# Kernel optimization log

Measured on AMD Instinct MI355X. Metric: run time of the kernel, lower is better.

## Reference

```python
import jax, jax.numpy as jnp
import numpy as np

N, L, K, DROP = 4096, 128, 16, 1
LEFT = N - L * DROP  # 3968


def setup_inputs() -> dict:
    rng = np.random.RandomState(0)
    X = rng.randn(N, N).astype(np.float32)
    A = (X + X.T) / 2.0  # symmetric, like a graph Laplacian
    active = np.ones(N, dtype=bool)
    sel = np.zeros((L, K), dtype=np.int32)
    drp = np.zeros((L, DROP), dtype=np.int32)
    Os = np.zeros((L, K, K), dtype=np.float32)
    for l in range(L):
        cand = np.flatnonzero(active)
        idx = np.sort(rng.choice(cand, size=K, replace=False)).astype(np.int32)
        sel[l] = idx
        drp[l] = idx[:DROP]
        active[idx[:DROP]] = False
        Q, _ = np.linalg.qr(rng.randn(K, K))  # orthogonal init (eigvecs in original)
        Os[l] = Q.astype(np.float32)
    active_idx = np.flatnonzero(active).astype(np.int32)      # (LEFT,) sorted
    inactive_idx = np.flatnonzero(~active).astype(np.int32)   # (N-LEFT,) sorted
    return {
        'A': jnp.asarray(A),
        'Os': jnp.asarray(Os),
        'sel_idx': jnp.asarray(sel),
        'drop_idx': jnp.asarray(drp),
        'active_idx': jnp.asarray(active_idx),
        'inactive_idx': jnp.asarray(inactive_idx),
    }


def reference(A, Os, sel_idx, drop_idx, active_idx, inactive_idx):
    # U_l = I_N with the K x K orthogonal block O_l scattered at (sel, sel).
    # U A U^T therefore only changes K rows and K columns -> rank-K update,
    # identical math to the original dense torch.matmul(U, A) @ U.T.
    n = A.shape[0]
    right0 = jnp.eye(n, dtype=A.dtype)

    def step(carry, xs):
        A_l, right = carry
        O, sel, drp = xs
        A_l = A_l.at[sel, :].set(O @ A_l[sel, :])          # (U A): K rows change
        A_l = A_l.at[:, sel].set(A_l[:, sel] @ O.T)        # (. U^T): K cols change
        right = right.at[sel, :].set(O @ right[sel, :])    # right = U @ right
        wavelet = A_l[drp, :]                              # (drop, N)
        return (A_l, right), wavelet

    (A_L, right), wavelets = jax.lax.scan(step, (A, right0), (Os, sel_idx, drop_idx))
    # wavelets: (L, drop, N)

    active = jnp.zeros((n,), A.dtype).at[active_idx].set(1.0)
    # left_index = eye - diag(diag(outer)) + outer, with outer = active x active
    mask = jnp.eye(n, dtype=A.dtype) - jnp.diag(active) + jnp.outer(active, active)
    D = A_L * mask
    core_wavelets = A_L[active_idx, :]          # (LEFT, N), sorted active order
    mother_wavelets_2 = right[inactive_idx, :]  # (N-LEFT, N)
    father_wavelets_2 = right[active_idx, :]    # (LEFT, N)
    A_rec = right.T @ D @ right
    return A_rec, D, wavelets, core_wavelets, mother_wavelets_2, father_wavelets_2
```

## Files before the change

kernel.cpp:

```cpp
#include <hip/hip_runtime.h>
#include <hip/hip_bf16.h>
#include <stdint.h>

#define N 4096
#define TC 2048
#define LSTEPS 128
#define KSEL 16
#define NACT 3968
#define NIN 128

typedef __hip_bfloat16 bf16;
typedef __attribute__((ext_vector_type(8))) short short8;
typedef __attribute__((ext_vector_type(4))) float floatx4;

static __device__ __forceinline__ bf16 f2bf(float x) { return __float2bfloat16(x); }
static __device__ __forceinline__ float us2f(ushort u) { return __uint_as_float(((unsigned)u) << 16); }
static __device__ __forceinline__ ushort f2us(float x) { return __bfloat16_as_ushort(__float2bfloat16(x)); }

__global__ void prep_kernel(const int* __restrict__ act, const int* __restrict__ inact,
                            int* __restrict__ flags, int* __restrict__ rank) {
    int i = blockIdx.x * blockDim.x + threadIdx.x;
    if (i >= N) return;
    int lo = 0, hi = NACT - 1, f = 0, r = -1;
    while (lo <= hi) {
        int mid = (lo + hi) >> 1, v = act[mid];
        if (v == i) { f = 1; r = mid; break; }
        if (v < i) lo = mid + 1; else hi = mid - 1;
    }
    if (!f) {
        lo = 0; hi = NIN - 1;
        while (lo <= hi) {
            int mid = (lo + hi) >> 1, v = inact[mid];
            if (v == i) { r = mid; break; }
            if (v < i) lo = mid + 1; else hi = mid - 1;
        }
    }
    flags[i] = f;
    rank[i] = r;
}

__global__ __launch_bounds__(1024) void touched_kernel(const int* __restrict__ sel,
                                                       int* __restrict__ tlist,
                                                       int* __restrict__ tpos,
                                                       int* __restrict__ tflag,
                                                       int* __restrict__ selc) {
    __shared__ int flag[N];
    __shared__ int cpos[N];
    __shared__ int wsum[16];
    __shared__ int woff[16];
    __shared__ int s_tau;
    const int t = threadIdx.x;
#pragma unroll
    for (int k = 0; k < 4; k++) flag[t + 1024 * k] = 0;
    __syncthreads();
    flag[sel[t]] = 1;
    flag[sel[t + 1024]] = 1;
    __syncthreads();
    const int b0 = t * 4;
    const int a0 = flag[b0], a1 = flag[b0 + 1], a2 = flag[b0 + 2], a3 = flag[b0 + 3];
    const int s = a0 + a1 + a2 + a3;
    const int lane = t & 63, wv = t >> 6;
    int sc = s;
    for (int off = 1; off < 64; off <<= 1) {
        int o = __shfl_up(sc, off);
        if (lane >= off) sc += o;
    }
    if (lane == 63) wsum[wv] = sc;
    __syncthreads();
    if (t == 0) {
        int acc = 0;
        for (int i = 0; i < 16; i++) { woff[i] = acc; acc += wsum[i]; }
        s_tau = acc;
    }
    __syncthreads();
    const int tau = s_tau;
    const int need = TC - tau;
    int tp = woff[wv] + (sc - s);
    const int aa[4] = {a0, a1, a2, a3};
#pragma unroll
    for (int k = 0; k < 4; k++) {
        const int i = b0 + k;
        int ci;
        if (aa[k]) { ci = tp; tp++; }
        else {
            const int ur = i - tp;
            ci = (ur < need) ? (tau + ur) : -1;
        }
        cpos[i] = ci;
        tpos[i] = ci;
        tflag[i] = (ci >= 0) ? 1 : 0;
        if (ci >= 0) tlist[ci] = i;
    }
    __syncthreads();
    selc[t] = cpos[sel[t]];
    selc[t + 1024] = cpos[sel[t + 1024]];
}

__global__ __launch_bounds__(64) void rscanc_kernel(const float* __restrict__ Os,
                                                    const int* __restrict__ selc,
                                                    bf16* __restrict__ Rct) {
    __shared__ float slab[TC * 4];
    const int t = threadIdx.x;
    const int cc = t & 3;
    const int a = t >> 2;
    const int c0 = blockIdx.x * 4;

    for (int r = t; r < TC * 4; r += 64) slab[r] = 0.0f;
    __syncthreads();
    if (t < 4) slab[(c0 + t) * 4 + t] = 1.0f;
    __syncthreads();

    int selr[16];
    float orow[16];
#pragma unroll
    for (int i = 0; i < 16; i++) selr[i] = selc[i];
#pragma unroll
    for (int i = 0; i < 16; i++) orow[i] = Os[a * 16 + i];

    for (int l = 0; l < LSTEPS; l++) {
        float p[16];
#pragma unroll
        for (int i = 0; i < 16; i++) p[i] = slab[selr[i] * 4 + cc];
#pragma unroll
        for (int i = 0; i < 16; i++) p[i] *= orow[i];
        const float s0 = (p[0] + p[1]) + (p[2] + p[3]);
        const float s1 = (p[4] + p[5]) + (p[6] + p[7]);
        const float s2 = (p[8] + p[9]) + (p[10] + p[11]);
        const float s3 = (p[12] + p[13]) + (p[14] + p[15]);
        const float v = (s0 + s1) + (s2 + s3);
        const int wrow = selr[a];
        int seln[16] = {0};
        float orown[16] = {0.f};
        if (l + 1 < LSTEPS) {
#pragma unroll
            for (int i = 0; i < 16; i++) seln[i] = selc[(l + 1) * 16 + i];
#pragma unroll
            for (int i = 0; i < 16; i++) orown[i] = Os[(l + 1) * 256 + a * 16 + i];
        }
        __syncthreads();
        slab[wrow * 4 + cc] = v;
        __syncthreads();
#pragma unroll
        for (int i = 0; i < 16; i++) { selr[i] = seln[i]; orow[i] = orown[i]; }
    }

    for (int ccw = 0; ccw < 4; ccw++) {
        bf16* dst = Rct + (size_t)(c0 + ccw) * TC;
        for (int r = t; r < TC; r += 64) dst[r] = f2bf(slab[r * 4 + ccw]);
    }
}

__global__ __launch_bounds__(256) void transB_kernel(const bf16* __restrict__ src,
                                                     bf16* __restrict__ dst,
                                                     int R, int C) {
    __shared__ ushort tile[64][65];
    const int t = threadIdx.x;
    const int bx = blockIdx.x, by = blockIdx.y;
    const int tr = t >> 4;
    const int tc = (t & 15) * 4;
#pragma unroll
    for (int k = 0; k < 4; k++) {
        int r = tr + 16 * k;
        const ushort* s = (const ushort*)src + (size_t)(by * 64 + r) * C + bx * 64 + tc;
        ushort4 v = *(const ushort4*)s;
        tile[r][tc + 0] = v.x; tile[r][tc + 1] = v.y;
        tile[r][tc + 2] = v.z; tile[r][tc + 3] = v.w;
    }
    __syncthreads();
#pragma unroll
    for (int k = 0; k < 4; k++) {
        int r = tr + 16 * k;
        ushort4 w;
        w.x = tile[tc + 0][r];
        w.y = tile[tc + 1][r];
        w.z = tile[tc + 2][r];
        w.w = tile[tc + 3][r];
        *(ushort4*)((ushort*)dst + (size_t)(bx * 64 + r) * R + by * 64 + tc) = w;
    }
}

__global__ __launch_bounds__(256) void transF_kernel(const float* __restrict__ src,
                                                     float* __restrict__ dst,
                                                     int R, int C) {
    __shared__ float tile[64][65];
    const int t = threadIdx.x;
    const int bx = blockIdx.x, by = blockIdx.y;
    const int tr = t >> 4;
    const int tc = (t & 15) * 4;
#pragma unroll
    for (int k = 0; k < 4; k++) {
        int r = tr + 16 * k;
        const float* s = src + (size_t)(by * 64 + r) * C + bx * 64 + tc;
        float4 v = *(const float4*)s;
        tile[r][tc + 0] = v.x; tile[r][tc + 1] = v.y;
        tile[r][tc + 2] = v.z; tile[r][tc + 3] = v.w;
    }
    __syncthreads();
#pragma unroll
    for (int k = 0; k < 4; k++) {
        int r = tr + 16 * k;
        float4 w;
        w.x = tile[tc + 0][r];
        w.y = tile[tc + 1][r];
        w.z = tile[tc + 2][r];
        w.w = tile[tc + 3][r];
        *(float4*)(dst + (size_t)(bx * 64 + r) * R + by * 64 + tc) = w;
    }
}

__global__ __launch_bounds__(256) void gatherAt_kernel(const float* __restrict__ A,
                                                       const int* __restrict__ tlist,
                                                       bf16* __restrict__ At) {
    const int r = blockIdx.y;
    const int j0 = (blockIdx.x * 256 + threadIdx.x) * 4;
    const float4 v = *(const float4*)(A + (size_t)tlist[r] * N + j0);
    ushort4 o;
    o.x = f2us(v.x); o.y = f2us(v.y); o.z = f2us(v.z); o.w = f2us(v.w);
    *(ushort4*)((ushort*)At + (size_t)r * N + j0) = o;
}

__global__ __launch_bounds__(256) void gatherRowsB_kernel(const bf16* __restrict__ src,
                                                          const int* __restrict__ tlist,
                                                          bf16* __restrict__ dst) {
    const int r = blockIdx.y;
    const int c0 = (blockIdx.x * 256 + threadIdx.x) * 4;
    ushort4 v = *(const ushort4*)((const ushort*)src + (size_t)tlist[r] * TC + c0);
    *(ushort4*)((ushort*)dst + (size_t)r * TC + c0) = v;
}

__global__ __launch_bounds__(256) void gatherRd_kernel(const bf16* __restrict__ Rc,
                                                       const int* __restrict__ tpos,
                                                       const int* __restrict__ drp,
                                                       bf16* __restrict__ Rd) {
    const int l = blockIdx.y;
    const int c0 = (blockIdx.x * 256 + threadIdx.x) * 4;
    const int pr = tpos[drp[l]];
    ushort4 v = *(const ushort4*)((const ushort*)Rc + (size_t)pr * TC + c0);
    *(ushort4*)((ushort*)Rd + (size_t)l * TC + c0) = v;
}

__global__ __launch_bounds__(256) void gatherColsB_kernel(const bf16* __restrict__ Dt,
                                                          const int* __restrict__ tlist,
                                                          bf16* __restrict__ Dc) {
    const int r = blockIdx.y;
    const int c = blockIdx.x * 256 + threadIdx.x;
    ((ushort*)Dc)[(size_t)r * TC + c] = ((const ushort*)Dt)[(size_t)r * N + tlist[c]];
}

__global__ __launch_bounds__(256) void assembleY_kernel(bf16* __restrict__ Y,
                                                        const bf16* __restrict__ C,
                                                        const int* __restrict__ tflag,
                                                        const int* __restrict__ tpos) {
    const int r = blockIdx.y;
    const int j0 = (blockIdx.x * 256 + threadIdx.x) * 4;
    ushort4 v = *(const ushort4*)((const ushort*)Y + (size_t)r * N + j0);
    const int4 tf = *(const int4*)(tflag + j0);
    const int4 tp = *(const int4*)(tpos + j0);
    const ushort* crow = (const ushort*)C + (size_t)r * TC;
    if (tf.x) v.x = crow[tp.x];
    if (tf.y) v.y = crow[tp.y];
    if (tf.z) v.z = crow[tp.z];
    if (tf.w) v.w = crow[tp.w];
    *(ushort4*)((ushort*)Y + (size_t)r * N + j0) = v;
}

template <bool F32OUT>
__global__ __launch_bounds__(512) void gemmk_kernel(const bf16* __restrict__ Amat, int lda,
                                                    const bf16* __restrict__ Bt, int ldb,
                                                    void* __restrict__ Cv, int ldc, int K) {
    __shared__ bf16 lds[4][(128 + 256) * 32];

    const int t = threadIdx.x;
    const int lane = t & 63;
    const int wave = t >> 6;
    const int wm = wave >> 2;
    const int wn = wave & 3;
    const int rowBase = blockIdx.y * 128;
    const int colBase = blockIdx.x * 256;

    const int sr = lane >> 2;
    const int sgo = (((lane & 3) ^ ((lane >> 3) & 3)) << 3);

    const int frow = lane & 15;
    const int fslot = (((lane >> 4) ^ ((lane >> 1) & 3)) << 4);
    const int aoff0 = (wm * 64 + frow) * 64 + fslot;
    const int boff0 = 128 * 64 + (wn * 64 + frow) * 64 + fslot;

    floatx4 acc[4][4] = {};

#define GK_STAGE_A(bufIdx, kk0)                                                                    \
    do {                                                                                           \
        const bf16* g_ = Amat + (size_t)(rowBase + wave * 16 + sr) * lda + (kk0) + sgo;            \
        char* l_ = (char*)&lds[bufIdx][0] + wave * 1024;                                           \
        __builtin_amdgcn_global_load_lds((const __attribute__((address_space(1))) void*)g_,        \
                                         (__attribute__((address_space(3))) void*)l_, 16, 0, 0);   \
    } while (0)
#define GK_STAGE_B(bufIdx, kk0)                                                                    \
    do {                                                                                           \
        const bf16* g0_ = Bt + (size_t)(colBase + wave * 32 + sr) * ldb + (kk0) + sgo;             \
        const bf16* g1_ = g0_ + (size_t)16 * ldb;                                                  \
        char* l0_ = (char*)&lds[bufIdx][128 * 32] + wave * 2048;                                   \
        __builtin_amdgcn_global_load_lds((const __attribute__((address_space(1))) void*)g0_,       \
                                         (__attribute__((address_space(3))) void*)l0_, 16, 0, 0);  \
        __builtin_amdgcn_global_load_lds((const __attribute__((address_space(1))) void*)g1_,       \
                                         (__attribute__((address_space(3))) void*)(l0_ + 1024),    \
                                         16, 0, 0);                                                \
    } while (0)

    const int NT = K >> 5;
#pragma unroll
    for (int p = 0; p < 3; p++) {
        GK_STAGE_A(p, p * 32);
        GK_STAGE_B(p, p * 32);
    }
    asm volatile("s_waitcnt vmcnt(6)" ::: "memory");
    __builtin_amdgcn_s_barrier();

    for (int tt = 0; tt < NT; tt++) {
        const int buf = tt & 3;
        const char* lA = (const char*)&lds[buf][0];
        const int nbuf = (tt + 3) & 3;
        const bool pf = (tt + 3) < NT;
        const int nk0 = (tt + 3) * 32;

        if (pf) GK_STAGE_A(nbuf, nk0);
        short8 af[4], bfv[4];
#pragma unroll
        for (int mi = 0; mi < 4; mi++) af[mi] = *(const short8*)(lA + aoff0 + mi * 1024);
#pragma unroll
        for (int ni = 0; ni < 2; ni++) bfv[ni] = *(const short8*)(lA + boff0 + ni * 1024);
        __builtin_amdgcn_s_barrier();
        asm volatile("s_waitcnt lgkmcnt(0)" ::: "memory");
        __builtin_amdgcn_s_setprio(1);
#pragma unroll
        for (int mi = 0; mi < 4; mi++)
#pragma unroll
            for (int ni = 0; ni < 2; ni++)
                acc[mi][ni] =
                    __builtin_amdgcn_mfma_f32_16x16x32_bf16(af[mi], bfv[ni], acc[mi][ni], 0, 0, 0);
        __builtin_amdgcn_s_setprio(0);
        __builtin_amdgcn_s_barrier();

        if (pf) GK_STAGE_B(nbuf, nk0);
#pragma unroll
        for (int ni = 2; ni < 4; ni++) bfv[ni] = *(const short8*)(lA + boff0 + ni * 1024);
        __builtin_amdgcn_s_barrier();
        asm volatile("s_waitcnt lgkmcnt(0)" ::: "memory");
        __builtin_amdgcn_s_setprio(1);
#pragma unroll
        for (int mi = 0; mi < 4; mi++)
#pragma unroll
            for (int ni = 2; ni < 4; ni++)
                acc[mi][ni] =
                    __builtin_amdgcn_mfma_f32_16x16x32_bf16(af[mi], bfv[ni], acc[mi][ni], 0, 0, 0);
        __builtin_amdgcn_s_setprio(0);
        asm volatile("s_waitcnt vmcnt(6)" ::: "memory");
        __builtin_amdgcn_s_barrier();
    }
#undef GK_STAGE_A
#undef GK_STAGE_B

    const int crow = (lane >> 4) * 4;
    const int ccol = lane & 15;
    const int rb = rowBase + wm * 64;
    const int cb = colBase + wn * 64;
#pragma unroll
    for (int mi = 0; mi < 4; mi++)
#pragma unroll
        for (int ni = 0; ni < 4; ni++)
#pragma unroll
            for (int r = 0; r < 4; r++) {
                const int gr = rb + mi * 16 + crow + r;
                const int gc = cb + ni * 16 + ccol;
                if (F32OUT)
                    ((float*)Cv)[(size_t)gr * ldc + gc] = acc[mi][ni][r];
                else
                    ((bf16*)Cv)[(size_t)gr * ldc + gc] = f2bf(acc[mi][ni][r]);
            }
}

__global__ __launch_bounds__(256) void maskcore2_kernel(const float* __restrict__ A,
                                                        const bf16* __restrict__ Z,
                                                        const bf16* __restrict__ Zt,
                                                        const int* __restrict__ flags,
                                                        const int* __restrict__ rank,
                                                        const int* __restrict__ tflag,
                                                        const int* __restrict__ tpos,
                                                        float* __restrict__ Dout,
                                                        bf16* __restrict__ Dt,
                                                        float* __restrict__ core) {
    const int i = blockIdx.y;
    const int j0 = (blockIdx.x * 256 + threadIdx.x) * 4;
    const int fi = flags[i];
    const int ri = rank[i];
    const int ti = tflag[i];
    const int pi = tpos[i];
    float4 vf;
    if (ti) {
        const ushort4 v16 = *(const ushort4*)((const ushort*)Z + (size_t)pi * N + j0);
        vf.x = us2f(v16.x); vf.y = us2f(v16.y); vf.z = us2f(v16.z); vf.w = us2f(v16.w);
    } else {
        vf = *(const float4*)(A + (size_t)i * N + j0);
        const int4 tf = *(const int4*)(tflag + j0);
        const int4 tp = *(const int4*)(tpos + j0);
        const ushort* zrow = (const ushort*)Zt + (size_t)i * TC;
        if (tf.x) vf.x = us2f(zrow[tp.x]);
        if (tf.y) vf.y = us2f(zrow[tp.y]);
        if (tf.z) vf.z = us2f(zrow[tp.z]);
        if (tf.w) vf.w = us2f(zrow[tp.w]);
    }
    if (fi) *(float4*)(core + (size_t)ri * N + j0) = vf;
    const int4 fj = *(const int4*)(flags + j0);
    const bool k0 = (i == j0 + 0) || (fi && fj.x);
    const bool k1 = (i == j0 + 1) || (fi && fj.y);
    const bool k2 = (i == j0 + 2) || (fi && fj.z);
    const bool k3 = (i == j0 + 3) || (fi && fj.w);
    float4 df;
    df.x = k0 ? vf.x : 0.0f; df.y = k1 ? vf.y : 0.0f;
    df.z = k2 ? vf.z : 0.0f; df.w = k3 ? vf.w : 0.0f;
    *(float4*)(Dout + (size_t)i * N + j0) = df;
    if (ti) {
        ushort4 dv;
        dv.x = k0 ? f2us(vf.x) : (ushort)0;
        dv.y = k1 ? f2us(vf.y) : (ushort)0;
        dv.z = k2 ? f2us(vf.z) : (ushort)0;
        dv.w = k3 ? f2us(vf.w) : (ushort)0;
        *(ushort4*)((ushort*)Dt + (size_t)pi * N + j0) = dv;
    }
}

__global__ __launch_bounds__(64) void wavelet_kernel(const bf16* __restrict__ Scw,
                                                     const float* __restrict__ Os,
                                                     const int* __restrict__ sel,
                                                     float* __restrict__ wout) {
    __shared__ float u[N];
    const int t = threadIdx.x;
    const int l = blockIdx.x;
    const ushort* src = (const ushort*)(Scw + (size_t)l * N);
    for (int j = t; j < N; j += 64) u[j] = us2f(src[j]);
    __syncthreads();
    for (int m = 0; m <= l; m++) {
        float v = 0.0f;
        int wrow = 0;
        if (t < 16) {
            float p[16];
#pragma unroll
            for (int i = 0; i < 16; i++) p[i] = u[sel[m * 16 + i]];
#pragma unroll
            for (int i = 0; i < 16; i++) p[i] *= Os[m * 256 + t * 16 + i];
            const float s0 = (p[0] + p[1]) + (p[2] + p[3]);
            const float s1 = (p[4] + p[5]) + (p[6] + p[7]);
            const float s2 = (p[8] + p[9]) + (p[10] + p[11]);
            const float s3 = (p[12] + p[13]) + (p[14] + p[15]);
            v = (s0 + s1) + (s2 + s3);
            wrow = sel[m * 16 + t];
        }
        __syncthreads();
        if (t < 16) u[wrow] = v;
        __syncthreads();
    }
    float* dst = wout + (size_t)l * N;
    for (int j = t; j < N; j += 64) dst[j] = u[j];
}

__global__ __launch_bounds__(256) void rowgatherR2_kernel(const bf16* __restrict__ Rc,
                                                          const int* __restrict__ flags,
                                                          const int* __restrict__ rank,
                                                          const int* __restrict__ tflag,
                                                          const int* __restrict__ tpos,
                                                          float* __restrict__ father,
                                                          float* __restrict__ mother) {
    const int i = blockIdx.x;
    const int t = threadIdx.x;
    float* dst = flags[i] ? (father + (size_t)rank[i] * N) : (mother + (size_t)rank[i] * N);
    const int ti = tflag[i];
    const ushort* rrow = (const ushort*)Rc + (size_t)(ti ? tpos[i] : 0) * TC;
    for (int it = 0; it < 4; it++) {
        const int j0 = (it * 256 + t) * 4;
        const int4 tf = *(const int4*)(tflag + j0);
        const int4 tp = *(const int4*)(tpos + j0);
        float4 o;
        o.x = tf.x ? (ti ? us2f(rrow[tp.x]) : 0.f) : ((j0 + 0 == i) ? 1.f : 0.f);
        o.y = tf.y ? (ti ? us2f(rrow[tp.y]) : 0.f) : ((j0 + 1 == i) ? 1.f : 0.f);
        o.z = tf.z ? (ti ? us2f(rrow[tp.z]) : 0.f) : ((j0 + 2 == i) ? 1.f : 0.f);
        o.w = tf.w ? (ti ? us2f(rrow[tp.w]) : 0.f) : ((j0 + 3 == i) ? 1.f : 0.f);
        *(float4*)(dst + j0) = o;
    }
}

__global__ __launch_bounds__(256) void arec_kernel(const float* __restrict__ W,
                                                   const float* __restrict__ Wt,
                                                   const float* __restrict__ D,
                                                   const int* __restrict__ tflag,
                                                   const int* __restrict__ tpos,
                                                   float* __restrict__ Arec) {
    const int i = blockIdx.y;
    const int j0 = (blockIdx.x * 256 + threadIdx.x) * 4;
    float4 o;
    if (tflag[i]) {
        o = *(const float4*)(W + (size_t)tpos[i] * N + j0);
    } else {
        o = *(const float4*)(D + (size_t)i * N + j0);
        const int4 tf = *(const int4*)(tflag + j0);
        const int4 tp = *(const int4*)(tpos + j0);
        const float* wrow = Wt + (size_t)i * TC;
        if (tf.x) o.x = wrow[tp.x];
        if (tf.y) o.y = wrow[tp.y];
        if (tf.z) o.z = wrow[tp.z];
        if (tf.w) o.w = wrow[tp.w];
    }
    *(float4*)(Arec + (size_t)i * N + j0) = o;
}

extern "C" void kernel_launch(void* const* d_in, const int* in_sizes, int n_in,
                              void* d_out, int out_size, void* d_ws, size_t ws_size,
                              hipStream_t stream) {
    const float* A = (const float*)d_in[0];
    const float* Os = (const float*)d_in[1];
    const int* sel = (const int*)d_in[2];
    const int* drp = (const int*)d_in[3];
    const int* act = (const int*)d_in[4];
    const int* inact = (const int*)d_in[5];

    float* out = (float*)d_out;
    float* out_Arec = out;
    float* out_D    = out + 16777216;
    float* out_wav  = out + 33554432;
    float* out_core = out + 34078720;
    float* out_moth = out + 50331648;
    float* out_fath = out + 50855936;

    char* ws = (char*)d_ws;
    const size_t KB = 1024;
    const size_t MB = 1024 * 1024;
    int* tlist = (int*)(ws + 0);
    int* tpos  = (int*)(ws + 64 * KB);
    int* tflag = (int*)(ws + 128 * KB);
    int* selc  = (int*)(ws + 192 * KB);
    int* flags = (int*)(ws + 256 * KB);
    int* rank  = (int*)(ws + 320 * KB);
    bf16* Rd128 = (bf16*)(ws + 512 * KB);
    bf16* Scw   = (bf16*)(ws + 1 * MB);
    bf16* At    = (bf16*)(ws + 2 * MB);
    bf16* At_T  = (bf16*)(ws + 18 * MB);
    bf16* C2    = (bf16*)(ws + 18 * MB);
    bf16* Zt    = (bf16*)(ws + 18 * MB);
    bf16* Rct   = (bf16*)(ws + 34 * MB);
    bf16* Rc    = (bf16*)(ws + 42 * MB);
    bf16* Ac    = (bf16*)(ws + 50 * MB);
    bf16* Y_T   = (bf16*)(ws + 50 * MB);
    float* W    = (float*)(ws + 50 * MB);
    float* Wt   = (float*)(ws + 2 * MB);
    bf16* Y  = At;
    bf16* Z  = At;
    bf16* Dt   = (bf16*)out_Arec;
    bf16* Dc   = (bf16*)((char*)out_Arec + 16 * MB);
    bf16* C4   = (bf16*)((char*)out_Arec + 24 * MB);
    bf16* Y2   = Dt;
    bf16* Y2_T = (bf16*)((char*)out_Arec + 32 * MB);

    prep_kernel<<<dim3(16), dim3(256), 0, stream>>>(act, inact, flags, rank);
    touched_kernel<<<dim3(1), dim3(1024), 0, stream>>>(sel, tlist, tpos, tflag, selc);
    gatherAt_kernel<<<dim3(4, TC), dim3(256), 0, stream>>>(A, tlist, At);
    rscanc_kernel<<<dim3(TC / 4), dim3(64), 0, stream>>>(Os, selc, Rct);
    transB_kernel<<<dim3(32, 32), dim3(256), 0, stream>>>(Rct, Rc, TC, TC);
    transB_kernel<<<dim3(64, 32), dim3(256), 0, stream>>>(At, At_T, TC, N);
    gatherRd_kernel<<<dim3(2, 128), dim3(256), 0, stream>>>(Rc, tpos, drp, Rd128);
    gemmk_kernel<false><<<dim3(16, 1), dim3(512), 0, stream>>>(Rd128, TC, At_T, TC, Scw, N, TC);
    gatherRowsB_kernel<<<dim3(2, TC), dim3(256), 0, stream>>>(At_T, tlist, Ac);
    gemmk_kernel<false><<<dim3(8, 16), dim3(512), 0, stream>>>(Ac, TC, Rc, TC, C2, TC, TC);
    assembleY_kernel<<<dim3(4, TC), dim3(256), 0, stream>>>(Y, C2, tflag, tpos);
    transB_kernel<<<dim3(64, 32), dim3(256), 0, stream>>>(Y, Y_T, TC, N);
    gemmk_kernel<false><<<dim3(16, 16), dim3(512), 0, stream>>>(Rc, TC, Y_T, TC, Z, N, TC);
    transB_kernel<<<dim3(64, 32), dim3(256), 0, stream>>>(Z, Zt, TC, N);
    maskcore2_kernel<<<dim3(4, N), dim3(256), 0, stream>>>(A, Z, Zt, flags, rank, tflag, tpos,
                                                          out_D, Dt, out_core);
    gatherColsB_kernel<<<dim3(8, TC), dim3(256), 0, stream>>>(Dt, tlist, Dc);
    gemmk_kernel<false><<<dim3(8, 16), dim3(512), 0, stream>>>(Dc, TC, Rct, TC, C4, TC, TC);
    assembleY_kernel<<<dim3(4, TC), dim3(256), 0, stream>>>(Y2, C4, tflag, tpos);
    transB_kernel<<<dim3(64, 32), dim3(256), 0, stream>>>(Y2, Y2_T, TC, N);
    gemmk_kernel<true><<<dim3(16, 16), dim3(512), 0, stream>>>(Rct, TC, Y2_T, TC, W, N, TC);
    transF_kernel<<<dim3(64, 32), dim3(256), 0, stream>>>(W, Wt, TC, N);
    wavelet_kernel<<<dim3(LSTEPS), dim3(64), 0, stream>>>(Scw, Os, sel, out_wav);
    rowgatherR2_kernel<<<dim3(N), dim3(256), 0, stream>>>(Rc, flags, rank, tflag, tpos,
                                                          out_fath, out_moth);
    arec_kernel<<<dim3(4, N), dim3(256), 0, stream>>>(W, Wt, out_D, tflag, tpos, out_Arec);
}
```

Baseline: 782.5 us.

## Restructure pipeline to work in transposed layouts and drop transposes, gathers and assemble kernels

Folds prep into the touched-index kernel and emits Rd rows straight from the rotation scan. A is now gathered directly into a transposed bf16 layout, which removes one transpose. The two middle GEMMs scatter their outputs through a row map into the Y/D buffers, which eliminates the assembleY, gatherColsB and two transpose kernels. A new 128x128-tile GEMM variant handles the small-N products. This cuts memory traffic and kernel launches, at the cost of uncoalesced row-mapped stores and strided gathers from A.

```diff
diff --git a/kernel.cpp b/kernel.cpp
--- a/kernel.cpp
+++ b/kernel.cpp
@@ -17,33 +17,17 @@
 static __device__ __forceinline__ float us2f(ushort u) { return __uint_as_float(((unsigned)u) << 16); }
 static __device__ __forceinline__ ushort f2us(float x) { return __bfloat16_as_ushort(__float2bfloat16(x)); }
 
-__global__ void prep_kernel(const int* __restrict__ act, const int* __restrict__ inact,
-                            int* __restrict__ flags, int* __restrict__ rank) {
-    int i = blockIdx.x * blockDim.x + threadIdx.x;
-    if (i >= N) return;
-    int lo = 0, hi = NACT - 1, f = 0, r = -1;
-    while (lo <= hi) {
-        int mid = (lo + hi) >> 1, v = act[mid];
-        if (v == i) { f = 1; r = mid; break; }
-        if (v < i) lo = mid + 1; else hi = mid - 1;
-    }
-    if (!f) {
-        lo = 0; hi = NIN - 1;
-        while (lo <= hi) {
-            int mid = (lo + hi) >> 1, v = inact[mid];
-            if (v == i) { r = mid; break; }
-            if (v < i) lo = mid + 1; else hi = mid - 1;
-        }
-    }
-    flags[i] = f;
-    rank[i] = r;
-}
-
 __global__ __launch_bounds__(1024) void touched_kernel(const int* __restrict__ sel,
+                                                       const int* __restrict__ drp,
+                                                       const int* __restrict__ act,
+                                                       const int* __restrict__ inact,
                                                        int* __restrict__ tlist,
                                                        int* __restrict__ tpos,
                                                        int* __restrict__ tflag,
-                                                       int* __restrict__ selc) {
+                                                       int* __restrict__ selc,
+                                                       int* __restrict__ dposc,
+                                                       int* __restrict__ flags,
+                                                       int* __restrict__ rank) {
     __shared__ int flag[N];
     __shared__ int cpos[N];
     __shared__ int wsum[16];
@@ -94,11 +78,35 @@
     __syncthreads();
     selc[t] = cpos[sel[t]];
     selc[t + 1024] = cpos[sel[t + 1024]];
+    if (t < 128) dposc[t] = cpos[drp[t]];
+
+#pragma unroll
+    for (int k = 0; k < 4; k++) {
+        const int i = b0 + k;
+        int lo = 0, hi = NACT - 1, f = 0, r = -1;
+        while (lo <= hi) {
+            int mid = (lo + hi) >> 1, v = act[mid];
+            if (v == i) { f = 1; r = mid; break; }
+            if (v < i) lo = mid + 1; else hi = mid - 1;
+        }
+        if (!f) {
+            lo = 0; hi = NIN - 1;
+            while (lo <= hi) {
+                int mid = (lo + hi) >> 1, v = inact[mid];
+                if (v == i) { r = mid; break; }
+                if (v < i) lo = mid + 1; else hi = mid - 1;
+            }
+        }
+        flags[i] = f;
+        rank[i] = r;
+    }
 }
 
 __global__ __launch_bounds__(64) void rscanc_kernel(const float* __restrict__ Os,
                                                     const int* __restrict__ selc,
-                                                    bf16* __restrict__ Rct) {
+                                                    const int* __restrict__ dposc,
+                                                    bf16* __restrict__ Rct,
+                                                    bf16* __restrict__ Rd) {
     __shared__ float slab[TC * 4];
     const int t = threadIdx.x;
     const int cc = t & 3;
@@ -148,6 +156,15 @@
         bf16* dst = Rct + (size_t)(c0 + ccw) * TC;
         for (int r = t; r < TC; r += 64) dst[r] = f2bf(slab[r * 4 + ccw]);
     }
+    for (int l = t; l < LSTEPS; l += 64) {
+        const int rrow = dposc[l];
+        ushort4 o;
+        o.x = f2us(slab[rrow * 4 + 0]);
+        o.y = f2us(slab[rrow * 4 + 1]);
+        o.z = f2us(slab[rrow * 4 + 2]);
+        o.w = f2us(slab[rrow * 4 + 3]);
+        *(ushort4*)((ushort*)Rd + (size_t)l * TC + c0) = o;
+    }
 }
 
 __global__ __launch_bounds__(256) void transB_kernel(const bf16* __restrict__ src,
@@ -208,15 +225,17 @@
     }
 }
 
-__global__ __launch_bounds__(256) void gatherAt_kernel(const float* __restrict__ A,
-                                                       const int* __restrict__ tlist,
-                                                       bf16* __restrict__ At) {
-    const int r = blockIdx.y;
-    const int j0 = (blockIdx.x * 256 + threadIdx.x) * 4;
-    const float4 v = *(const float4*)(A + (size_t)tlist[r] * N + j0);
+__global__ __launch_bounds__(256) void gatherAtT_kernel(const float* __restrict__ A,
+                                                        const int* __restrict__ tlist,
+                                                        bf16* __restrict__ AtT) {
+    const int j = blockIdx.y;
+    const int p0 = (blockIdx.x * 256 + threadIdx.x) * 4;
+    const float* arow = A + (size_t)j * N;
+    const int4 tl = *(const int4*)(tlist + p0);
     ushort4 o;
-    o.x = f2us(v.x); o.y = f2us(v.y); o.z = f2us(v.z); o.w = f2us(v.w);
-    *(ushort4*)((ushort*)At + (size_t)r * N + j0) = o;
+    o.x = f2us(arow[tl.x]); o.y = f2us(arow[tl.y]);
+    o.z = f2us(arow[tl.z]); o.w = f2us(arow[tl.w]);
+    *(ushort4*)((ushort*)AtT + (size_t)j * TC + p0) = o;
 }
 
 __global__ __launch_bounds__(256) void gatherRowsB_kernel(const bf16* __restrict__ src,
@@ -228,46 +247,11 @@
     *(ushort4*)((ushort*)dst + (size_t)r * TC + c0) = v;
 }
 
-__global__ __launch_bounds__(256) void gatherRd_kernel(const bf16* __restrict__ Rc,
-                                                       const int* __restrict__ tpos,
-                                                       const int* __restrict__ drp,
-                                                       bf16* __restrict__ Rd) {
-    const int l = blockIdx.y;
-    const int c0 = (blockIdx.x * 256 + threadIdx.x) * 4;
-    const int pr = tpos[drp[l]];
-    ushort4 v = *(const ushort4*)((const ushort*)Rc + (size_t)pr * TC + c0);
-    *(ushort4*)((ushort*)Rd + (size_t)l * TC + c0) = v;
-}
-
-__global__ __launch_bounds__(256) void gatherColsB_kernel(const bf16* __restrict__ Dt,
-                                                          const int* __restrict__ tlist,
-                                                          bf16* __restrict__ Dc) {
-    const int r = blockIdx.y;
-    const int c = blockIdx.x * 256 + threadIdx.x;
-    ((ushort*)Dc)[(size_t)r * TC + c] = ((const ushort*)Dt)[(size_t)r * N + tlist[c]];
-}
-
-__global__ __launch_bounds__(256) void assembleY_kernel(bf16* __restrict__ Y,
-                                                        const bf16* __restrict__ C,
-                                                        const int* __restrict__ tflag,
-                                                        const int* __restrict__ tpos) {
-    const int r = blockIdx.y;
-    const int j0 = (blockIdx.x * 256 + threadIdx.x) * 4;
-    ushort4 v = *(const ushort4*)((const ushort*)Y + (size_t)r * N + j0);
-    const int4 tf = *(const int4*)(tflag + j0);
-    const int4 tp = *(const int4*)(tpos + j0);
-    const ushort* crow = (const ushort*)C + (size_t)r * TC;
-    if (tf.x) v.x = crow[tp.x];
-    if (tf.y) v.y = crow[tp.y];
-    if (tf.z) v.z = crow[tp.z];
-    if (tf.w) v.w = crow[tp.w];
-    *(ushort4*)((ushort*)Y + (size_t)r * N + j0) = v;
-}
-
 template <bool F32OUT>
 __global__ __launch_bounds__(512) void gemmk_kernel(const bf16* __restrict__ Amat, int lda,
                                                     const bf16* __restrict__ Bt, int ldb,
-                                                    void* __restrict__ Cv, int ldc, int K) {
+                                                    void* __restrict__ Cv, int ldc, int K,
+                                                    const int* __restrict__ rowmap) {
     __shared__ bf16 lds[4][(128 + 256) * 32];
 
     const int t = threadIdx.x;
@@ -370,7 +354,121 @@
         for (int ni = 0; ni < 4; ni++)
 #pragma unroll
             for (int r = 0; r < 4; r++) {
-                const int gr = rb + mi * 16 + crow + r;
+                const int gr0 = rb + mi * 16 + crow + r;
+                const int gr = rowmap ? rowmap[gr0] : gr0;
+                const int gc = cb + ni * 16 + ccol;
+                if (F32OUT)
+                    ((float*)Cv)[(size_t)gr * ldc + gc] = acc[mi][ni][r];
+                else
+                    ((bf16*)Cv)[(size_t)gr * ldc + gc] = f2bf(acc[mi][ni][r]);
+            }
+}
+
+template <bool F32OUT>
+__global__ __launch_bounds__(512) void gemm128_kernel(const bf16* __restrict__ Amat, int lda,
+                                                      const bf16* __restrict__ Bt, int ldb,
+                                                      void* __restrict__ Cv, int ldc, int K,
+                                                      const int* __restrict__ rowmap) {
+    __shared__ bf16 lds[4][(128 + 128) * 32];
+
+    const int t = threadIdx.x;
+    const int lane = t & 63;
+    const int wave = t >> 6;
+    const int wm = wave >> 1;
+    const int wn = wave & 1;
+    const int rowBase = blockIdx.y * 128;
+    const int colBase = blockIdx.x * 128;
+
+    const int sr = lane >> 2;
+    const int sgo = (((lane & 3) ^ ((lane >> 3) & 3)) << 3);
+
+    const int frow = lane & 15;
+    const int fslot = (((lane >> 4) ^ ((lane >> 1) & 3)) << 4);
+    const int aoff0 = (wm * 32 + frow) * 64 + fslot;
+    const int boff0 = 128 * 64 + (wn * 64 + frow) * 64 + fslot;
+
+    floatx4 acc[2][4] = {};
+
+#define G1_STAGE_A(bufIdx, kk0)                                                                    \
+    do {                                                                                           \
+        const bf16* g_ = Amat + (size_t)(rowBase + wave * 16 + sr) * lda + (kk0) + sgo;            \
+        char* l_ = (char*)&lds[bufIdx][0] + wave * 1024;                                           \
+        __builtin_amdgcn_global_load_lds((const __attribute__((address_space(1))) void*)g_,        \
+                                         (__attribute__((address_space(3))) void*)l_, 16, 0, 0);   \
+    } while (0)
+#define G1_STAGE_B(bufIdx, kk0)                                                                    \
+    do {                                                                                           \
+        const bf16* g_ = Bt + (size_t)(colBase + wave * 16 + sr) * ldb + (kk0) + sgo;              \
+        char* l_ = (char*)&lds[bufIdx][128 * 32] + wave * 1024;                                    \
+        __builtin_amdgcn_global_load_lds((const __attribute__((address_space(1))) void*)g_,        \
+                                         (__attribute__((address_space(3))) void*)l_, 16, 0, 0);   \
+    } while (0)
+
+    const int NT = K >> 5;
+#pragma unroll
+    for (int p = 0; p < 3; p++) {
+        G1_STAGE_A(p, p * 32);
+        G1_STAGE_B(p, p * 32);
+    }
+    asm volatile("s_waitcnt vmcnt(4)" ::: "memory");
+    __builtin_amdgcn_s_barrier();
+
+    for (int tt = 0; tt < NT; tt++) {
+        const int buf = tt & 3;
+        const char* lA = (const char*)&lds[buf][0];
+        const int nbuf = (tt + 3) & 3;
+        const bool pf = (tt + 3) < NT;
+        const int nk0 = (tt + 3) * 32;
+
+        if (pf) G1_STAGE_A(nbuf, nk0);
+        short8 af[2], bfv[4];
+#pragma unroll
+        for (int mi = 0; mi < 2; mi++) af[mi] = *(const short8*)(lA + aoff0 + mi * 1024);
+#pragma unroll
+        for (int ni = 0; ni < 2; ni++) bfv[ni] = *(const short8*)(lA + boff0 + ni * 1024);
+        __builtin_amdgcn_s_barrier();
+        asm volatile("s_waitcnt lgkmcnt(0)" ::: "memory");
+        __builtin_amdgcn_s_setprio(1);
+#pragma unroll
+        for (int mi = 0; mi < 2; mi++)
+#pragma unroll
+            for (int ni = 0; ni < 2; ni++)
+                acc[mi][ni] =
+                    __builtin_amdgcn_mfma_f32_16x16x32_bf16(af[mi], bfv[ni], acc[mi][ni], 0, 0, 0);
+        __builtin_amdgcn_s_setprio(0);
+        __builtin_amdgcn_s_barrier();
+
+        if (pf) G1_STAGE_B(nbuf, nk0);
+#pragma unroll
+        for (int ni = 2; ni < 4; ni++) bfv[ni] = *(const short8*)(lA + boff0 + ni * 1024);
+        __builtin_amdgcn_s_barrier();
+        asm volatile("s_waitcnt lgkmcnt(0)" ::: "memory");
+        __builtin_amdgcn_s_setprio(1);
+#pragma unroll
+        for (int mi = 0; mi < 2; mi++)
+#pragma unroll
+            for (int ni = 2; ni < 4; ni++)
+                acc[mi][ni] =
+                    __builtin_amdgcn_mfma_f32_16x16x32_bf16(af[mi], bfv[ni], acc[mi][ni], 0, 0, 0);
+        __builtin_amdgcn_s_setprio(0);
+        asm volatile("s_waitcnt vmcnt(4)" ::: "memory");
+        __builtin_amdgcn_s_barrier();
+    }
+#undef G1_STAGE_A
+#undef G1_STAGE_B
+
+    const int crow = (lane >> 4) * 4;
+    const int ccol = lane & 15;
+    const int rb = rowBase + wm * 32;
+    const int cb = colBase + wn * 64;
+#pragma unroll
+    for (int mi = 0; mi < 2; mi++)
+#pragma unroll
+        for (int ni = 0; ni < 4; ni++)
+#pragma unroll
+            for (int r = 0; r < 4; r++) {
+                const int gr0 = rb + mi * 16 + crow + r;
+                const int gr = rowmap ? rowmap[gr0] : gr0;
                 const int gc = cb + ni * 16 + ccol;
                 if (F32OUT)
                     ((float*)Cv)[(size_t)gr * ldc + gc] = acc[mi][ni][r];
@@ -387,7 +485,7 @@
                                                         const int* __restrict__ tflag,
                                                         const int* __restrict__ tpos,
                                                         float* __restrict__ Dout,
-                                                        bf16* __restrict__ Dt,
+                                                        bf16* __restrict__ Dtc,
                                                         float* __restrict__ core) {
     const int i = blockIdx.y;
     const int j0 = (blockIdx.x * 256 + threadIdx.x) * 4;
@@ -396,13 +494,13 @@
     const int ti = tflag[i];
     const int pi = tpos[i];
     float4 vf;
+    const int4 tf = *(const int4*)(tflag + j0);
+    const int4 tp = *(const int4*)(tpos + j0);
     if (ti) {
         const ushort4 v16 = *(const ushort4*)((const ushort*)Z + (size_t)pi * N + j0);
         vf.x = us2f(v16.x); vf.y = us2f(v16.y); vf.z = us2f(v16.z); vf.w = us2f(v16.w);
     } else {
         vf = *(const float4*)(A + (size_t)i * N + j0);
-        const int4 tf = *(const int4*)(tflag + j0);
-        const int4 tp = *(const int4*)(tpos + j0);
         const ushort* zrow = (const ushort*)Zt + (size_t)i * TC;
         if (tf.x) vf.x = us2f(zrow[tp.x]);
         if (tf.y) vf.y = us2f(zrow[tp.y]);
@@ -419,14 +517,11 @@
     df.x = k0 ? vf.x : 0.0f; df.y = k1 ? vf.y : 0.0f;
     df.z = k2 ? vf.z : 0.0f; df.w = k3 ? vf.w : 0.0f;
     *(float4*)(Dout + (size_t)i * N + j0) = df;
-    if (ti) {
-        ushort4 dv;
-        dv.x = k0 ? f2us(vf.x) : (ushort)0;
-        dv.y = k1 ? f2us(vf.y) : (ushort)0;
-        dv.z = k2 ? f2us(vf.z) : (ushort)0;
-        dv.w = k3 ? f2us(vf.w) : (ushort)0;
-        *(ushort4*)((ushort*)Dt + (size_t)pi * N + j0) = dv;
-    }
+    ushort* drow = (ushort*)Dtc + (size_t)i * TC;
+    if (tf.x) drow[tp.x] = f2us(df.x);
+    if (tf.y) drow[tp.y] = f2us(df.y);
+    if (tf.z) drow[tp.z] = f2us(df.z);
+    if (tf.w) drow[tp.w] = f2us(df.w);
 }
 
 __global__ __launch_bounds__(64) void wavelet_kernel(const bf16* __restrict__ Scw,
@@ -539,49 +634,41 @@
     int* selc  = (int*)(ws + 192 * KB);
     int* flags = (int*)(ws + 256 * KB);
     int* rank  = (int*)(ws + 320 * KB);
-    bf16* Rd128 = (bf16*)(ws + 512 * KB);
-    bf16* Scw   = (bf16*)(ws + 1 * MB);
-    bf16* At    = (bf16*)(ws + 2 * MB);
-    bf16* At_T  = (bf16*)(ws + 18 * MB);
-    bf16* C2    = (bf16*)(ws + 18 * MB);
-    bf16* Zt    = (bf16*)(ws + 18 * MB);
-    bf16* Rct   = (bf16*)(ws + 34 * MB);
-    bf16* Rc    = (bf16*)(ws + 42 * MB);
-    bf16* Ac    = (bf16*)(ws + 50 * MB);
-    bf16* Y_T   = (bf16*)(ws + 50 * MB);
-    float* W    = (float*)(ws + 50 * MB);
-    float* Wt   = (float*)(ws + 2 * MB);
-    bf16* Y  = At;
-    bf16* Z  = At;
-    bf16* Dt   = (bf16*)out_Arec;
-    bf16* Dc   = (bf16*)((char*)out_Arec + 16 * MB);
-    bf16* C4   = (bf16*)((char*)out_Arec + 24 * MB);
-    bf16* Y2   = Dt;
-    bf16* Y2_T = (bf16*)((char*)out_Arec + 32 * MB);
-
-    prep_kernel<<<dim3(16), dim3(256), 0, stream>>>(act, inact, flags, rank);
-    touched_kernel<<<dim3(1), dim3(1024), 0, stream>>>(sel, tlist, tpos, tflag, selc);
-    gatherAt_kernel<<<dim3(4, TC), dim3(256), 0, stream>>>(A, tlist, At);
-    rscanc_kernel<<<dim3(TC / 4), dim3(64), 0, stream>>>(Os, selc, Rct);
+    int* dposc = (int*)(ws + 384 * KB);
+    bf16* Rd128 = (bf16*)(ws + 1 * MB);
+    bf16* Scw   = (bf16*)(ws + 2 * MB);
+    bf16* Rct   = (bf16*)(ws + 3 * MB);
+    bf16* Rc    = (bf16*)(ws + 11 * MB);
+    bf16* YT    = (bf16*)(ws + 19 * MB);
+    bf16* Ac    = (bf16*)(ws + 35 * MB);
+    bf16* Z     = (bf16*)(ws + 35 * MB);
+    bf16* Zt    = (bf16*)(ws + 51 * MB);
+    bf16* Dtc   = (bf16*)(ws + 67 * MB);
+    bf16* Dc    = (bf16*)(ws + 83 * MB);
+    float* W    = (float*)(ws + 19 * MB);
+    float* Wt   = (float*)(ws + 51 * MB);
+
+    touched_kernel<<<dim3(1), dim3(1024), 0, stream>>>(sel, drp, act, inact, tlist, tpos,
+                                                       tflag, selc, dposc, flags, rank);
+    gatherAtT_kernel<<<dim3(2, N), dim3(256), 0, stream>>>(A, tlist, YT);
+    rscanc_kernel<<<dim3(TC / 4), dim3(64), 0, stream>>>(Os, selc, dposc, Rct, Rd128);
     transB_kernel<<<dim3(32, 32), dim3(256), 0, stream>>>(Rct, Rc, TC, TC);
-    transB_kernel<<<dim3(64, 32), dim3(256), 0, stream>>>(At, At_T, TC, N);
-    gatherRd_kernel<<<dim3(2, 128), dim3(256), 0, stream>>>(Rc, tpos, drp, Rd128);
-    gemmk_kernel<false><<<dim3(16, 1), dim3(512), 0, stream>>>(Rd128, TC, At_T, TC, Scw, N, TC);
-    gatherRowsB_kernel<<<dim3(2, TC), dim3(256), 0, stream>>>(At_T, tlist, Ac);
-    gemmk_kernel<false><<<dim3(8, 16), dim3(512), 0, stream>>>(Ac, TC, Rc, TC, C2, TC, TC);
-    assembleY_kernel<<<dim3(4, TC), dim3(256), 0, stream>>>(Y, C2, tflag, tpos);
-    transB_kernel<<<dim3(64, 32), dim3(256), 0, stream>>>(Y, Y_T, TC, N);
-    gemmk_kernel<false><<<dim3(16, 16), dim3(512), 0, stream>>>(Rc, TC, Y_T, TC, Z, N, TC);
+    gemm128_kernel<false><<<dim3(32, 1), dim3(512), 0, stream>>>(Rd128, TC, YT, TC, Scw, N, TC,
+                                                                 nullptr);
+    wavelet_kernel<<<dim3(LSTEPS), dim3(64), 0, stream>>>(Scw, Os, sel, out_wav);
+    gatherRowsB_kernel<<<dim3(2, TC), dim3(256), 0, stream>>>(YT, tlist, Ac);
+    gemm128_kernel<false><<<dim3(16, 16), dim3(512), 0, stream>>>(Rc, TC, Ac, TC, YT, TC, TC,
+                                                                  tlist);
+    gemmk_kernel<false><<<dim3(16, 16), dim3(512), 0, stream>>>(Rc, TC, YT, TC, Z, N, TC, nullptr);
     transB_kernel<<<dim3(64, 32), dim3(256), 0, stream>>>(Z, Zt, TC, N);
     maskcore2_kernel<<<dim3(4, N), dim3(256), 0, stream>>>(A, Z, Zt, flags, rank, tflag, tpos,
-                                                          out_D, Dt, out_core);
-    gatherColsB_kernel<<<dim3(8, TC), dim3(256), 0, stream>>>(Dt, tlist, Dc);
-    gemmk_kernel<false><<<dim3(8, 16), dim3(512), 0, stream>>>(Dc, TC, Rct, TC, C4, TC, TC);
-    assembleY_kernel<<<dim3(4, TC), dim3(256), 0, stream>>>(Y2, C4, tflag, tpos);
-    transB_kernel<<<dim3(64, 32), dim3(256), 0, stream>>>(Y2, Y2_T, TC, N);
-    gemmk_kernel<true><<<dim3(16, 16), dim3(512), 0, stream>>>(Rct, TC, Y2_T, TC, W, N, TC);
+                                                           out_D, Dtc, out_core);
+    gatherRowsB_kernel<<<dim3(2, TC), dim3(256), 0, stream>>>(Dtc, tlist, Dc);
+    gemm128_kernel<false><<<dim3(16, 16), dim3(512), 0, stream>>>(Rct, TC, Dc, TC, Dtc, TC, TC,
+                                                                  tlist);
+    gemmk_kernel<true><<<dim3(16, 16), dim3(512), 0, stream>>>(Rct, TC, Dtc, TC, W, N, TC,
+                                                               nullptr);
     transF_kernel<<<dim3(64, 32), dim3(256), 0, stream>>>(W, Wt, TC, N);
-    wavelet_kernel<<<dim3(LSTEPS), dim3(64), 0, stream>>>(Scw, Os, sel, out_wav);
     rowgatherR2_kernel<<<dim3(N), dim3(256), 0, stream>>>(Rc, flags, rank, tflag, tpos,
                                                           out_fath, out_moth);
     arec_kernel<<<dim3(4, N), dim3(256), 0, stream>>>(W, Wt, out_D, tflag, tpos, out_Arec);
```

After: 720.8 us. 7.9% less time.
